# Kernel tuning notes

Measured on AMD Instinct MI355X. Metric: run time of the kernel, lower is better.

Reference implementation:

```python
import jax, jax.numpy as jnp
import numpy as np

B, S, E = 8, 2048, 768
N, H = 12, 64
INIT = 0.02
IGNORE = -100000.0


def setup_inputs() -> dict:
    key = jax.random.key(0)
    ks = jax.random.split(key, 5)
    return {
        "normalized_resid_pre": jax.random.normal(ks[0], (B, S, E), jnp.float32),
        "W_Q": jax.random.normal(ks[1], (N, E, H), jnp.float32) * INIT,
        "W_K": jax.random.normal(ks[2], (N, E, H), jnp.float32) * INIT,
        "W_V": jax.random.normal(ks[3], (N, E, H), jnp.float32) * INIT,
        "W_O": jax.random.normal(ks[4], (N, H, E), jnp.float32) * INIT,
        "b_Q": jnp.zeros((N, H), jnp.float32),
        "b_K": jnp.zeros((N, H), jnp.float32),
        "b_V": jnp.zeros((N, H), jnp.float32),
        "b_O": jnp.zeros((E,), jnp.float32),
    }


def reference(normalized_resid_pre, W_Q, W_K, W_V, W_O, b_Q, b_K, b_V, b_O):
    x = normalized_resid_pre
    b, s, e = x.shape
    d_head = W_Q.shape[-1]
    q = jnp.einsum('bse,neh->bsnh', x, W_Q) + b_Q  # [b, sq, n, h]
    k = jnp.einsum('bse,neh->bsnh', x, W_K) + b_K
    v = jnp.einsum('bse,neh->bsnh', x, W_V) + b_V
    scores = jnp.einsum('bqnh,bknh->bnqk', q, k) / jnp.sqrt(jnp.float32(d_head))
    mask = jnp.tril(jnp.ones((s, s), jnp.float32))  # [sq, sk]
    masked = mask * scores + (1.0 - mask) * IGNORE
    probs = jax.nn.softmax(masked, axis=-1)
    z = jnp.einsum('bnqk,bknh->bqnh', probs, v)
    # sum over heads of per-head output projection + bias
    out = jnp.einsum('bqnh,nhe->bqe', z, W_O) + b_O
    return out
```

## Files before the change

kernel.cpp:

```cpp
#include <hip/hip_runtime.h>
#include <hip/hip_bf16.h>
#include <stdint.h>


#define B_ 8
#define S_ 2048
#define E_ 768
#define NHEADS 12
#define HD 64
#define BS (B_*S_)
#define NHD (NHEADS*HD)

typedef short bf16x8 __attribute__((ext_vector_type(8)));
typedef short bf16x4 __attribute__((ext_vector_type(4)));
typedef float f32x4  __attribute__((ext_vector_type(4)));
typedef __hip_bfloat16 bf16;

typedef const __attribute__((address_space(1))) char* as1_t;
typedef __attribute__((address_space(3))) char* as3_t;

__device__ __forceinline__ f32x4 mfma16(bf16x8 a, bf16x8 b, f32x4 c) {
    return __builtin_amdgcn_mfma_f32_16x16x32_bf16(a, b, c, 0, 0, 0);
}
__device__ __forceinline__ bf16x8 ld8(const bf16* p) {
    return *reinterpret_cast<const bf16x8*>(p);
}
__device__ __forceinline__ void gload16(const bf16* g, bf16* l) {
    __builtin_amdgcn_global_load_lds((as1_t)g, (as3_t)l, 16, 0, 0);
}
__device__ __forceinline__ bf16x8 pack8(f32x4 a, f32x4 b) {
    union { bf16x8 v; __hip_bfloat162 h[4]; } u;
    u.h[0] = __float22bfloat162_rn(make_float2(a[0], a[1]));
    u.h[1] = __float22bfloat162_rn(make_float2(a[2], a[3]));
    u.h[2] = __float22bfloat162_rn(make_float2(b[0], b[1]));
    u.h[3] = __float22bfloat162_rn(make_float2(b[2], b[3]));
    return u.v;
}

__global__ __launch_bounds__(256) void prep_kernel(
    const float* __restrict__ x,  const float* __restrict__ Wq,
    const float* __restrict__ Wk, const float* __restrict__ Wv,
    const float* __restrict__ Wo,
    bf16* __restrict__ xb,  bf16* __restrict__ WqT, bf16* __restrict__ WkT,
    bf16* __restrict__ WvT, bf16* __restrict__ WoT)
{
    const int tid = blockIdx.x * 256 + threadIdx.x;
    const int nth = gridDim.x * 256;
    for (int i = tid; i < BS*E_; i += nth)
        xb[i] = __float2bfloat16(x[i]);
    for (int i = tid; i < NHD*E_; i += nth) {
        const int c = i / E_;
        const int e = i - c*E_;
        const int n = c >> 6, h = c & 63;
        const int src = (n*E_ + e)*HD + h;
        WqT[i] = __float2bfloat16(Wq[src]);
        WkT[i] = __float2bfloat16(Wk[src]);
        WvT[i] = __float2bfloat16(Wv[src]);
        WoT[e*NHD + c] = __float2bfloat16(Wo[i]);
    }
}


#define FENCE() asm volatile("" ::: "memory")
#define VMCNT3() asm volatile("s_waitcnt vmcnt(3)" ::: "memory")

#define A_ELEM(kh, rg) (((kh)*16 + (rg))*512)
#define B_ELEM(kh, rg) (((kh)*12 + (rg))*512)

#define STG_A(dst, gbase, kt, kh) do {                                            \
    const bf16* _s = (gbase) + (size_t)(l16)*768 + (kt)*64 + (kh)*32 + quad*8;    \
    gload16(_s + (size_t)(w*16)*768,     &(dst)[A_ELEM(kh, w)]);                  \
    gload16(_s + (size_t)((w+8)*16)*768, &(dst)[A_ELEM(kh, w+8)]);                \
} while (0)

#define STG_B(dst, gbase, kt) do {                                                \
    const bf16* _s = (gbase) + (size_t)(l16)*768 + (kt)*64 + quad*8;              \
    const int _k1 = (w < 4) ? 0 : 1;                                              \
    const int _r1 = (w < 4) ? (w + 8) : (w - 4);                                  \
    gload16(_s + (size_t)(w*16)*768,        &(dst)[B_ELEM(0, w)]);                \
    gload16(_s + (size_t)(_r1*16)*768 + _k1*32, &(dst)[B_ELEM(_k1, _r1)]);        \
    gload16(_s + (size_t)((w+4)*16)*768 + 32,   &(dst)[B_ELEM(1, w+4)]);          \
} while (0)

#define PHASE(bufA, bufB, q, LOADB, STAGE, WAIT) do {                             \
    if (LOADB) {                                                                  \
        _Pragma("unroll") for (int n = 0; n < 3; ++n)                             \
        _Pragma("unroll") for (int ks = 0; ks < 2; ++ks)                          \
            bfr[n][ks] = ld8(&(bufB)[((ks)*12 + wn*3 + n)*512 + lane*8]);         \
    }                                                                             \
    bf16x8 afr[2][2];                                                             \
    _Pragma("unroll") for (int m = 0; m < 2; ++m)                                 \
    _Pragma("unroll") for (int ks = 0; ks < 2; ++ks)                              \
        afr[m][ks] = ld8(&(bufA)[((ks)*16 + wm*8 + (q)*2 + m)*512 + lane*8]);     \
    STAGE;                                                                        \
    FENCE(); __builtin_amdgcn_s_barrier(); FENCE();                               \
    asm volatile("s_waitcnt lgkmcnt(0)" ::: "memory");                            \
    __builtin_amdgcn_s_setprio(1);                                                \
    _Pragma("unroll") for (int m = 0; m < 2; ++m)                                 \
    _Pragma("unroll") for (int n = 0; n < 3; ++n)                                 \
    _Pragma("unroll") for (int ks = 0; ks < 2; ++ks)                              \
        acc[(q)*2 + m][n] = mfma16(afr[m][ks], bfr[n][ks], acc[(q)*2 + m][n]);    \
    __builtin_amdgcn_s_setprio(0);                                                \
    WAIT;                                                                         \
    FENCE(); __builtin_amdgcn_s_barrier(); FENCE();                               \
} while (0)

#define GEMM192_BODY(Ab, Bb)                                                      \
    f32x4 acc[8][3];                                                              \
    _Pragma("unroll") for (int mf = 0; mf < 8; ++mf)                              \
    _Pragma("unroll") for (int nf = 0; nf < 3; ++nf)                              \
        acc[mf][nf] = (f32x4){0.f, 0.f, 0.f, 0.f};                                \
    bf16x8 bfr[3][2];                                                             \
    STG_A(sA0, Ab, 0, 0); STG_A(sA0, Ab, 0, 1);                                   \
    STG_B(sB0, Bb, 0);                                                            \
    STG_B(sB1, Bb, 1);                                                            \
    VMCNT3();                                                                     \
    FENCE(); __builtin_amdgcn_s_barrier(); FENCE();                               \
    _Pragma("unroll 1")                                                           \
    for (int i = 0; i < 6; ++i) {                                                 \
        const int kA  = 2*i + 1;                                                  \
        const int kN  = (2*i + 2 < 12) ? 2*i + 2 : 11;                            \
        const int kN3 = (2*i + 3 < 12) ? 2*i + 3 : 11;                            \
        PHASE(sA0, sB0, 0, 1, STG_A(sA1, Ab, kA, 0), (void)0);                    \
        PHASE(sA0, sB0, 1, 0, STG_A(sA1, Ab, kA, 1), (void)0);                    \
        PHASE(sA0, sB0, 2, 0, STG_B(sB0, Bb, kN),    (void)0);                    \
        PHASE(sA0, sB0, 3, 0, (void)0,               VMCNT3());                   \
        PHASE(sA1, sB1, 0, 1, STG_A(sA0, Ab, kN, 0), (void)0);                    \
        PHASE(sA1, sB1, 1, 0, STG_A(sA0, Ab, kN, 1), (void)0);                    \
        PHASE(sA1, sB1, 2, 0, STG_B(sB1, Bb, kN3),   (void)0);                    \
        PHASE(sA1, sB1, 3, 0, (void)0,               VMCNT3());                   \
    }                                                                             \
    asm volatile("s_waitcnt vmcnt(0)" ::: "memory");

__global__ __launch_bounds__(512, 2) void qkv_gemm256(
    const bf16* __restrict__ xb, const bf16* __restrict__ WT,
    const float* __restrict__ bq, const float* __restrict__ bk, const float* __restrict__ bv,
    bf16* __restrict__ Qb, bf16* __restrict__ Kb, bf16* __restrict__ VTb)
{
    __shared__ __align__(16) bf16 sA0[16384];
    __shared__ __align__(16) bf16 sA1[16384];
    __shared__ __align__(16) bf16 sB0[12288];
    __shared__ __align__(16) bf16 sB1[12288];

    const int tm = blockIdx.x, tn = blockIdx.y;
    const int lane = threadIdx.x & 63;
    const int w    = threadIdx.x >> 6;
    const int wm = w >> 2, wn = w & 3;
    const int l16 = lane & 15, quad = lane >> 4;
    const bf16* Ab = xb + (size_t)tm*256*E_;
    const bf16* Bb = WT + (size_t)tn*192*E_;

    GEMM192_BODY(Ab, Bb);

    const int mat = tn >> 2;
    const int cloc0 = (tn & 3)*192 + wn*48;
    const float* bias = (mat==0) ? bq : (mat==1) ? bk : bv;
    const float scale = (mat==0) ? 0.125f * 1.44269504088896340736f : 1.0f;
    bf16* dstQK = (mat==0) ? Qb : Kb;
    #pragma unroll
    for (int nf = 0; nf < 3; ++nf) {
        const int col = cloc0 + nf*16 + l16;
        const int hn = col >> 6, h = col & 63;
        const float bb = bias[col];
        #pragma unroll
        for (int mf = 0; mf < 8; ++mf) {
            const int row = tm*256 + wm*128 + mf*16 + quad*4;
            const int bi = row >> 11;
            const int s  = row & (S_-1);
            if (mat < 2) {
                bf16* d = dstQK + ((size_t)(bi*NHEADS + hn)*S_ + s)*HD + h;
                #pragma unroll
                for (int r = 0; r < 4; ++r)
                    d[(size_t)r*HD] = __float2bfloat16((acc[mf][nf][r] + bb)*scale);
            } else {
                bf16* d = VTb + ((size_t)(bi*NHEADS + hn)*HD + h)*S_ + s;
                union { bf16x4 v; bf16 e[4]; } u;
                #pragma unroll
                for (int r = 0; r < 4; ++r) u.e[r] = __float2bfloat16(acc[mf][nf][r] + bb);
                *reinterpret_cast<bf16x4*>(d) = u.v;
            }
        }
    }
}

__global__ __launch_bounds__(512, 2) void out_gemm256(
    const bf16* __restrict__ Z, const bf16* __restrict__ WoT,
    const float* __restrict__ bo, float* __restrict__ out)
{
    __shared__ __align__(16) bf16 sA0[16384];
    __shared__ __align__(16) bf16 sA1[16384];
    __shared__ __align__(16) bf16 sB0[12288];
    __shared__ __align__(16) bf16 sB1[12288];

    const int tm = blockIdx.x, tn = blockIdx.y;
    const int lane = threadIdx.x & 63;
    const int w    = threadIdx.x >> 6;
    const int wm = w >> 2, wn = w & 3;
    const int l16 = lane & 15, quad = lane >> 4;
    const bf16* Ab = Z   + (size_t)tm*256*NHD;
    const bf16* Bb = WoT + (size_t)tn*192*NHD;

    GEMM192_BODY(Ab, Bb);

    #pragma unroll
    for (int nf = 0; nf < 3; ++nf) {
        const int col = tn*192 + wn*48 + nf*16 + l16;
        const float bb = bo[col];
        #pragma unroll
        for (int mf = 0; mf < 8; ++mf) {
            const int row = tm*256 + wm*128 + mf*16 + quad*4;
            float* d = out + (size_t)row*E_ + col;
            #pragma unroll
            for (int r = 0; r < 4; ++r)
                d[(size_t)r*E_] = acc[mf][nf][r] + bb;
        }
    }
}

__global__ __launch_bounds__(256, 3) void attn_kernel(
    const bf16* __restrict__ Qb, const bf16* __restrict__ Kb,
    const bf16* __restrict__ VTb, bf16* __restrict__ Z)
{
    __shared__ __align__(16) bf16 sK[2][64*64];
    __shared__ __align__(16) bf16 sV[2][64*64];

    const int id = blockIdx.x;
    const int bx = id / 96;
    const int g  = id - bx*96;
    const int hn = g % NHEADS, b = g / NHEADS;
    const int tid  = threadIdx.x;
    const int w    = tid >> 6;
    const int lane = tid & 63;
    const int l16 = lane & 15, quad = lane >> 4;
    const size_t bn = (size_t)b*NHEADS + hn;

    const bf16* Qbase = Qb  + bn*S_*HD;
    const bf16* Kbase = Kb  + bn*S_*HD;
    const bf16* Vbase = VTb + bn*HD*S_;

    const int mA = tid, mB = tid + 256;
    const int rA = mA >> 3, cgA = mA & 7;
    const int rB = mB >> 3, cgB = mB & 7;
    const int slA = (rA*8 + ((cgA + rA + (rA>>3)) & 7)) * 8;
    const int slB = (rB*8 + ((cgB + rB + (rB>>3)) & 7)) * 8;
    const size_t vofA = (size_t)rA*S_ + cgA*8;
    const size_t vofB = (size_t)rB*S_ + cgB*8;

    const int kperm = (l16 >> 2)*8 + (l16 & 3);
    int kidx[2][2][2];
    #pragma unroll
    for (int c=0;c<2;c++)
        #pragma unroll
        for (int bg=0;bg<2;bg++)
            #pragma unroll
            for (int hf=0;hf<2;hf++) {
                const int r = 32*c + 4*bg + kperm;
                const int q = hf*4 + quad;
                kidx[c][bg][hf] = (r*8 + ((q + r + (r>>3)) & 7)) * 8;
            }
    int vidx[4][2];
    #pragma unroll
    for (int ht=0;ht<4;ht++)
        #pragma unroll
        for (int c=0;c<2;c++) {
            const int rho = ht*16 + l16;
            const int q = c*4 + quad;
            vidx[ht][c] = (rho*8 + ((q + rho + (rho>>3)) & 7)) * 8;
        }

    #pragma unroll
    for (int half = 0; half < 2; ++half) {
        const int qblk = half ? (S_/128 - 1 - bx) : bx;
        const int ktb  = 2*qblk + 1;
        const int ktw  = 2*qblk + (w >> 1);
        const int qbase = qblk*128 + w*32;

        bf16x8 bqf[2][2];
        #pragma unroll
        for (int qi=0;qi<2;qi++)
            #pragma unroll
            for (int hf=0;hf<2;hf++)
                bqf[qi][hf] = ld8(Qbase + (size_t)(qbase + qi*16 + l16)*HD + hf*32 + quad*8);

        f32x4 acc[2][4];
        #pragma unroll
        for (int qi=0;qi<2;qi++)
            #pragma unroll
            for (int ht=0;ht<4;ht++) acc[qi][ht] = (f32x4){0.f,0.f,0.f,0.f};
        float lsum[2] = {0.f, 0.f};

        bf16x8 k0 = ld8(Kbase + (size_t)mA*8);
        bf16x8 k1 = ld8(Kbase + (size_t)mB*8);
        bf16x8 v0 = ld8(Vbase + vofA);
        bf16x8 v1 = ld8(Vbase + vofB);
        *reinterpret_cast<bf16x8*>(&sK[0][slA]) = k0;
        *reinterpret_cast<bf16x8*>(&sK[0][slB]) = k1;
        *reinterpret_cast<bf16x8*>(&sV[0][slA]) = v0;
        *reinterpret_cast<bf16x8*>(&sV[0][slB]) = v1;
        __syncthreads();

        for (int kt = 0; kt <= ktb; ++kt) {
            if (kt < ktb) {
                const size_t kt1 = (size_t)(kt+1)*64;
                k0 = ld8(Kbase + kt1*HD + (size_t)mA*8);
                k1 = ld8(Kbase + kt1*HD + (size_t)mB*8);
                v0 = ld8(Vbase + vofA + kt1);
                v1 = ld8(Vbase + vofB + kt1);
            }
            if (kt <= ktw) {
                const bf16* kb = sK[kt & 1];
                const bf16* vb = sV[kt & 1];
                #pragma unroll
                for (int c=0;c<2;c++) {
                    const bf16x8 akA0 = ld8(kb + kidx[c][0][0]);
                    const bf16x8 akA1 = ld8(kb + kidx[c][0][1]);
                    const bf16x8 akB0 = ld8(kb + kidx[c][1][0]);
                    const bf16x8 akB1 = ld8(kb + kidx[c][1][1]);
                    bf16x8 av[4];
                    #pragma unroll
                    for (int ht=0;ht<4;ht++) av[ht] = ld8(vb + vidx[ht][c]);

                    #pragma unroll
                    for (int qi=0;qi<2;qi++) {
                        f32x4 s0 = (f32x4){0.f,0.f,0.f,0.f};
                        s0 = mfma16(akA0, bqf[qi][0], s0);
                        s0 = mfma16(akA1, bqf[qi][1], s0);
                        f32x4 s1 = (f32x4){0.f,0.f,0.f,0.f};
                        s1 = mfma16(akB0, bqf[qi][0], s1);
                        s1 = mfma16(akB1, bqf[qi][1], s1);
                        if (kt == ktw) {
                            const int q  = qbase + qi*16 + l16;
                            const int kb0 = kt*64 + c*32 + quad*8;
                            #pragma unroll
                            for (int r=0;r<4;r++) {
                                s0[r] = (kb0 + r     > q) ? -1e30f : s0[r];
                                s1[r] = (kb0 + 4 + r > q) ? -1e30f : s1[r];
                            }
                        }
                        float ls = 0.f;
                        #pragma unroll
                        for (int r=0;r<4;r++) {
                            s0[r] = __builtin_amdgcn_exp2f(s0[r]);
                            s1[r] = __builtin_amdgcn_exp2f(s1[r]);
                            ls += s0[r] + s1[r];
                        }
                        lsum[qi] += ls;
                        const bf16x8 pf = pack8(s0, s1);
                        #pragma unroll
                        for (int ht=0;ht<4;ht++)
                            acc[qi][ht] = mfma16(av[ht], pf, acc[qi][ht]);
                    }
                }
            }
            if (kt < ktb) {
                const int nb = (kt+1) & 1;
                *reinterpret_cast<bf16x8*>(&sK[nb][slA]) = k0;
                *reinterpret_cast<bf16x8*>(&sK[nb][slB]) = k1;
                *reinterpret_cast<bf16x8*>(&sV[nb][slA]) = v0;
                *reinterpret_cast<bf16x8*>(&sV[nb][slB]) = v1;
            }
            __syncthreads();
        }

        #pragma unroll
        for (int qi=0;qi<2;qi++) {
            float rs = lsum[qi];
            rs += __shfl_xor(rs, 16, 64);
            rs += __shfl_xor(rs, 32, 64);
            const float inv_l = 1.0f / rs;
            const int q = qbase + qi*16 + l16;
            bf16* zp = Z + ((size_t)b*S_ + q)*NHD + (size_t)hn*HD + quad*4;
            #pragma unroll
            for (int ht=0;ht<4;ht++) {
                union { bf16x4 v; bf16 e[4]; } u;
                #pragma unroll
                for (int r=0;r<4;r++) u.e[r] = __float2bfloat16(acc[qi][ht][r] * inv_l);
                *reinterpret_cast<bf16x4*>(zp + ht*16) = u.v;
            }
        }
    }
}

extern "C" void kernel_launch(void* const* d_in, const int* in_sizes, int n_in,
                              void* d_out, int out_size, void* d_ws, size_t ws_size,
                              hipStream_t stream)
{
    const float* x  = (const float*)d_in[0];
    const float* Wq = (const float*)d_in[1];
    const float* Wk = (const float*)d_in[2];
    const float* Wv = (const float*)d_in[3];
    const float* Wo = (const float*)d_in[4];
    const float* bq = (const float*)d_in[5];
    const float* bk = (const float*)d_in[6];
    const float* bv = (const float*)d_in[7];
    const float* bo = (const float*)d_in[8];
    float* out = (float*)d_out;

    char* ws = (char*)d_ws;
    size_t off = 0;
    auto alloc = [&](size_t bytes){ char* p = ws + off; off += (bytes + 255) & ~(size_t)255; return p; };
    bf16* xb  = (bf16*)alloc((size_t)BS*E_*2);
    bf16* WT  = (bf16*)alloc((size_t)3*NHD*E_*2);
    bf16* WoT = (bf16*)alloc((size_t)E_*NHD*2);
    bf16* Qb  = (bf16*)alloc((size_t)BS*NHD*2);
    bf16* Kb  = (bf16*)alloc((size_t)BS*NHD*2);
    bf16* VTb = (bf16*)alloc((size_t)BS*NHD*2);
    bf16* Zb  = (bf16*)alloc((size_t)BS*NHD*2);

    bf16* WqT = WT;
    bf16* WkT = WT + (size_t)NHD*E_;
    bf16* WvT = WT + (size_t)2*NHD*E_;

    prep_kernel<<<4096, 256, 0, stream>>>(x, Wq, Wk, Wv, Wo, xb, WqT, WkT, WvT, WoT);
    qkv_gemm256<<<dim3(BS/256, 12), 512, 0, stream>>>(xb, WT, bq, bk, bv, Qb, Kb, VTb);
    attn_kernel<<<768, 256, 0, stream>>>(Qb, Kb, VTb, Zb);
    out_gemm256<<<dim3(BS/256, E_/192), 512, 0, stream>>>(Zb, WoT, bo, out);
}
```

Before: 238.2 us.

## Triple-buffer A tiles in LDS to prefetch two K-steps ahead in GEMMs

```diff
diff --git a/kernel.cpp b/kernel.cpp
--- a/kernel.cpp
+++ b/kernel.cpp
@@ -62,7 +62,8 @@
 
 
 #define FENCE() asm volatile("" ::: "memory")
-#define VMCNT3() asm volatile("s_waitcnt vmcnt(3)" ::: "memory")
+#define VMCNT7() asm volatile("s_waitcnt vmcnt(7)" ::: "memory")
+#define MIN11(x) ((x) < 11 ? (x) : 11)
 
 #define A_ELEM(kh, rg) (((kh)*16 + (rg))*512)
 #define B_ELEM(kh, rg) (((kh)*12 + (rg))*512)
@@ -105,6 +106,16 @@
     FENCE(); __builtin_amdgcn_s_barrier(); FENCE();                               \
 } while (0)
 
+#define ITER8(r0, r1, w2, k0, Ab, Bb)                                             \
+    PHASE(r0, sB0, 0, 1, STG_A(w2, Ab, MIN11((k0)+2), 0), (void)0);               \
+    PHASE(r0, sB0, 1, 0, STG_A(w2, Ab, MIN11((k0)+2), 1), (void)0);               \
+    PHASE(r0, sB0, 2, 0, STG_B(sB0, Bb, MIN11((k0)+2)),   (void)0);               \
+    PHASE(r0, sB0, 3, 0, (void)0,                         VMCNT7());              \
+    PHASE(r1, sB1, 0, 1, STG_A(r0, Ab, MIN11((k0)+3), 0), (void)0);               \
+    PHASE(r1, sB1, 1, 0, STG_A(r0, Ab, MIN11((k0)+3), 1), (void)0);               \
+    PHASE(r1, sB1, 2, 0, STG_B(sB1, Bb, MIN11((k0)+3)),   (void)0);               \
+    PHASE(r1, sB1, 3, 0, (void)0,                         VMCNT7());
+
 #define GEMM192_BODY(Ab, Bb)                                                      \
     f32x4 acc[8][3];                                                              \
     _Pragma("unroll") for (int mf = 0; mf < 8; ++mf)                              \
@@ -113,22 +124,16 @@
     bf16x8 bfr[3][2];                                                             \
     STG_A(sA0, Ab, 0, 0); STG_A(sA0, Ab, 0, 1);                                   \
     STG_B(sB0, Bb, 0);                                                            \
+    STG_A(sA1, Ab, 1, 0); STG_A(sA1, Ab, 1, 1);                                   \
     STG_B(sB1, Bb, 1);                                                            \
-    VMCNT3();                                                                     \
+    VMCNT7();                                                                     \
     FENCE(); __builtin_amdgcn_s_barrier(); FENCE();                               \
     _Pragma("unroll 1")                                                           \
-    for (int i = 0; i < 6; ++i) {                                                 \
-        const int kA  = 2*i + 1;                                                  \
-        const int kN  = (2*i + 2 < 12) ? 2*i + 2 : 11;                            \
-        const int kN3 = (2*i + 3 < 12) ? 2*i + 3 : 11;                            \
-        PHASE(sA0, sB0, 0, 1, STG_A(sA1, Ab, kA, 0), (void)0);                    \
-        PHASE(sA0, sB0, 1, 0, STG_A(sA1, Ab, kA, 1), (void)0);                    \
-        PHASE(sA0, sB0, 2, 0, STG_B(sB0, Bb, kN),    (void)0);                    \
-        PHASE(sA0, sB0, 3, 0, (void)0,               VMCNT3());                   \
-        PHASE(sA1, sB1, 0, 1, STG_A(sA0, Ab, kN, 0), (void)0);                    \
-        PHASE(sA1, sB1, 1, 0, STG_A(sA0, Ab, kN, 1), (void)0);                    \
-        PHASE(sA1, sB1, 2, 0, STG_B(sB1, Bb, kN3),   (void)0);                    \
-        PHASE(sA1, sB1, 3, 0, (void)0,               VMCNT3());                   \
+    for (int ii = 0; ii < 2; ++ii) {                                              \
+        const int k0 = 6*ii;                                                      \
+        ITER8(sA0, sA1, sA2, k0+0, Ab, Bb)                                        \
+        ITER8(sA2, sA0, sA1, k0+2, Ab, Bb)                                        \
+        ITER8(sA1, sA2, sA0, k0+4, Ab, Bb)                                        \
     }                                                                             \
     asm volatile("s_waitcnt vmcnt(0)" ::: "memory");
 
@@ -139,6 +144,7 @@
 {
     __shared__ __align__(16) bf16 sA0[16384];
     __shared__ __align__(16) bf16 sA1[16384];
+    __shared__ __align__(16) bf16 sA2[16384];
     __shared__ __align__(16) bf16 sB0[12288];
     __shared__ __align__(16) bf16 sB1[12288];
 
@@ -189,6 +195,7 @@
 {
     __shared__ __align__(16) bf16 sA0[16384];
     __shared__ __align__(16) bf16 sA1[16384];
+    __shared__ __align__(16) bf16 sA2[16384];
     __shared__ __align__(16) bf16 sB0[12288];
     __shared__ __align__(16) bf16 sB1[12288];
 
```

Result: faster. 232.2 us (-2.5%).

## Shrink GEMM M-tile to 128 and simplify pipeline to per-k-tile double buffering

Applied to the files above, without the earlier changes.

```diff
diff --git a/kernel.cpp b/kernel.cpp
--- a/kernel.cpp
+++ b/kernel.cpp
@@ -62,15 +62,18 @@
 
 
 #define FENCE() asm volatile("" ::: "memory")
-#define VMCNT3() asm volatile("s_waitcnt vmcnt(3)" ::: "memory")
-
-#define A_ELEM(kh, rg) (((kh)*16 + (rg))*512)
+#define LGKM0() do { asm volatile("s_waitcnt lgkmcnt(0)" ::: "memory"); \
+                     __builtin_amdgcn_sched_barrier(0); } while (0)
+#define VMCNT0() asm volatile("s_waitcnt vmcnt(0)" ::: "memory")
+#define MIN11(x) ((x) < 11 ? (x) : 11)
+
+#define A_ELEM(kh, rg) (((kh)*8 + (rg))*512)
 #define B_ELEM(kh, rg) (((kh)*12 + (rg))*512)
 
-#define STG_A(dst, gbase, kt, kh) do {                                            \
-    const bf16* _s = (gbase) + (size_t)(l16)*768 + (kt)*64 + (kh)*32 + quad*8;    \
-    gload16(_s + (size_t)(w*16)*768,     &(dst)[A_ELEM(kh, w)]);                  \
-    gload16(_s + (size_t)((w+8)*16)*768, &(dst)[A_ELEM(kh, w+8)]);                \
+#define STG_A(dst, gbase, kt) do {                                                \
+    const bf16* _s = (gbase) + (size_t)(w*16 + l16)*768 + (kt)*64 + quad*8;       \
+    gload16(_s,      &(dst)[A_ELEM(0, w)]);                                       \
+    gload16(_s + 32, &(dst)[A_ELEM(1, w)]);                                       \
 } while (0)
 
 #define STG_B(dst, gbase, kt) do {                                                \
@@ -82,63 +85,67 @@
     gload16(_s + (size_t)((w+4)*16)*768 + 32,   &(dst)[B_ELEM(1, w+4)]);          \
 } while (0)
 
-#define PHASE(bufA, bufB, q, LOADB, STAGE, WAIT) do {                             \
-    if (LOADB) {                                                                  \
+#define KTILE(bufA, bufB, nA, nB, ktn, Ab, Bb) do {                               \
+                                          \
+    _Pragma("unroll") for (int n = 0; n < 3; ++n)                                 \
+    _Pragma("unroll") for (int ks = 0; ks < 2; ++ks)                              \
+        bfr[n][ks] = ld8(&(bufB)[((ks)*12 + wn*3 + n)*512 + lane*8]);             \
+    {                                                                             \
+        bf16x8 afr[2][2];                                                         \
+        _Pragma("unroll") for (int m = 0; m < 2; ++m)                             \
+        _Pragma("unroll") for (int ks = 0; ks < 2; ++ks)                          \
+            afr[m][ks] = ld8(&(bufA)[((ks)*8 + wm*4 + m)*512 + lane*8]);          \
+        STG_A(nA, Ab, ktn);                                                       \
+        LGKM0();                                                                  \
+        __builtin_amdgcn_s_setprio(1);                                            \
+        _Pragma("unroll") for (int m = 0; m < 2; ++m)                             \
         _Pragma("unroll") for (int n = 0; n < 3; ++n)                             \
         _Pragma("unroll") for (int ks = 0; ks < 2; ++ks)                          \
-            bfr[n][ks] = ld8(&(bufB)[((ks)*12 + wn*3 + n)*512 + lane*8]);         \
+            acc[m][n] = mfma16(afr[m][ks], bfr[n][ks], acc[m][n]);                \
+        __builtin_amdgcn_s_setprio(0);                                            \
     }                                                                             \
-    bf16x8 afr[2][2];                                                             \
-    _Pragma("unroll") for (int m = 0; m < 2; ++m)                                 \
-    _Pragma("unroll") for (int ks = 0; ks < 2; ++ks)                              \
-        afr[m][ks] = ld8(&(bufA)[((ks)*16 + wm*8 + (q)*2 + m)*512 + lane*8]);     \
-    STAGE;                                                                        \
-    FENCE(); __builtin_amdgcn_s_barrier(); FENCE();                               \
-    asm volatile("s_waitcnt lgkmcnt(0)" ::: "memory");                            \
-    __builtin_amdgcn_s_setprio(1);                                                \
-    _Pragma("unroll") for (int m = 0; m < 2; ++m)                                 \
-    _Pragma("unroll") for (int n = 0; n < 3; ++n)                                 \
-    _Pragma("unroll") for (int ks = 0; ks < 2; ++ks)                              \
-        acc[(q)*2 + m][n] = mfma16(afr[m][ks], bfr[n][ks], acc[(q)*2 + m][n]);    \
-    __builtin_amdgcn_s_setprio(0);                                                \
-    WAIT;                                                                         \
+                                                    \
+    {                                                                             \
+        bf16x8 afr[2][2];                                                         \
+        _Pragma("unroll") for (int m = 0; m < 2; ++m)                             \
+        _Pragma("unroll") for (int ks = 0; ks < 2; ++ks)                          \
+            afr[m][ks] = ld8(&(bufA)[((ks)*8 + wm*4 + 2 + m)*512 + lane*8]);      \
+        STG_B(nB, Bb, ktn);                                                       \
+        LGKM0();                                                                  \
+        __builtin_amdgcn_s_setprio(1);                                            \
+        _Pragma("unroll") for (int m = 0; m < 2; ++m)                             \
+        _Pragma("unroll") for (int n = 0; n < 3; ++n)                             \
+        _Pragma("unroll") for (int ks = 0; ks < 2; ++ks)                          \
+            acc[2+m][n] = mfma16(afr[m][ks], bfr[n][ks], acc[2+m][n]);            \
+        __builtin_amdgcn_s_setprio(0);                                            \
+    }                                                                             \
+    VMCNT0();                                                                     \
     FENCE(); __builtin_amdgcn_s_barrier(); FENCE();                               \
 } while (0)
 
-#define GEMM192_BODY(Ab, Bb)                                                      \
-    f32x4 acc[8][3];                                                              \
-    _Pragma("unroll") for (int mf = 0; mf < 8; ++mf)                              \
+#define GEMM128_BODY(Ab, Bb)                                                      \
+    f32x4 acc[4][3];                                                              \
+    _Pragma("unroll") for (int mf = 0; mf < 4; ++mf)                              \
     _Pragma("unroll") for (int nf = 0; nf < 3; ++nf)                              \
         acc[mf][nf] = (f32x4){0.f, 0.f, 0.f, 0.f};                                \
     bf16x8 bfr[3][2];                                                             \
-    STG_A(sA0, Ab, 0, 0); STG_A(sA0, Ab, 0, 1);                                   \
-    STG_B(sB0, Bb, 0);                                                            \
-    STG_B(sB1, Bb, 1);                                                            \
-    VMCNT3();                                                                     \
+    STG_A(sA0, Ab, 0); STG_B(sB0, Bb, 0);                                         \
+    VMCNT0();                                                                     \
     FENCE(); __builtin_amdgcn_s_barrier(); FENCE();                               \
     _Pragma("unroll 1")                                                           \
-    for (int i = 0; i < 6; ++i) {                                                 \
-        const int kA  = 2*i + 1;                                                  \
-        const int kN  = (2*i + 2 < 12) ? 2*i + 2 : 11;                            \
-        const int kN3 = (2*i + 3 < 12) ? 2*i + 3 : 11;                            \
-        PHASE(sA0, sB0, 0, 1, STG_A(sA1, Ab, kA, 0), (void)0);                    \
-        PHASE(sA0, sB0, 1, 0, STG_A(sA1, Ab, kA, 1), (void)0);                    \
-        PHASE(sA0, sB0, 2, 0, STG_B(sB0, Bb, kN),    (void)0);                    \
-        PHASE(sA0, sB0, 3, 0, (void)0,               VMCNT3());                   \
-        PHASE(sA1, sB1, 0, 1, STG_A(sA0, Ab, kN, 0), (void)0);                    \
-        PHASE(sA1, sB1, 1, 0, STG_A(sA0, Ab, kN, 1), (void)0);                    \
-        PHASE(sA1, sB1, 2, 0, STG_B(sB1, Bb, kN3),   (void)0);                    \
-        PHASE(sA1, sB1, 3, 0, (void)0,               VMCNT3());                   \
-    }                                                                             \
-    asm volatile("s_waitcnt vmcnt(0)" ::: "memory");
-
-__global__ __launch_bounds__(512, 2) void qkv_gemm256(
+    for (int i2 = 0; i2 < 6; ++i2) {                                              \
+        const int kt0 = 2*i2;                                                     \
+        KTILE(sA0, sB0, sA1, sB1, kt0 + 1,        Ab, Bb);                        \
+        KTILE(sA1, sB1, sA0, sB0, MIN11(kt0 + 2), Ab, Bb);                        \
+    }
+
+__global__ __launch_bounds__(512, 4) void qkv_gemm256(
     const bf16* __restrict__ xb, const bf16* __restrict__ WT,
     const float* __restrict__ bq, const float* __restrict__ bk, const float* __restrict__ bv,
     bf16* __restrict__ Qb, bf16* __restrict__ Kb, bf16* __restrict__ VTb)
 {
-    __shared__ __align__(16) bf16 sA0[16384];
-    __shared__ __align__(16) bf16 sA1[16384];
+    __shared__ __align__(16) bf16 sA0[8192];
+    __shared__ __align__(16) bf16 sA1[8192];
     __shared__ __align__(16) bf16 sB0[12288];
     __shared__ __align__(16) bf16 sB1[12288];
 
@@ -147,10 +154,10 @@
     const int w    = threadIdx.x >> 6;
     const int wm = w >> 2, wn = w & 3;
     const int l16 = lane & 15, quad = lane >> 4;
-    const bf16* Ab = xb + (size_t)tm*256*E_;
+    const bf16* Ab = xb + (size_t)tm*128*E_;
     const bf16* Bb = WT + (size_t)tn*192*E_;
 
-    GEMM192_BODY(Ab, Bb);
+    GEMM128_BODY(Ab, Bb);
 
     const int mat = tn >> 2;
     const int cloc0 = (tn & 3)*192 + wn*48;
@@ -163,8 +170,8 @@
         const int hn = col >> 6, h = col & 63;
         const float bb = bias[col];
         #pragma unroll
-        for (int mf = 0; mf < 8; ++mf) {
-            const int row = tm*256 + wm*128 + mf*16 + quad*4;
+        for (int mf = 0; mf < 4; ++mf) {
+            const int row = tm*128 + wm*64 + mf*16 + quad*4;
             const int bi = row >> 11;
             const int s  = row & (S_-1);
             if (mat < 2) {
@@ -183,12 +190,12 @@
     }
 }
 
-__global__ __launch_bounds__(512, 2) void out_gemm256(
+__global__ __launch_bounds__(512, 4) void out_gemm256(
     const bf16* __restrict__ Z, const bf16* __restrict__ WoT,
     const float* __restrict__ bo, float* __restrict__ out)
 {
-    __shared__ __align__(16) bf16 sA0[16384];
-    __shared__ __align__(16) bf16 sA1[16384];
+    __shared__ __align__(16) bf16 sA0[8192];
+    __shared__ __align__(16) bf16 sA1[8192];
     __shared__ __align__(16) bf16 sB0[12288];
     __shared__ __align__(16) bf16 sB1[12288];
 
@@ -197,18 +204,18 @@
     const int w    = threadIdx.x >> 6;
     const int wm = w >> 2, wn = w & 3;
     const int l16 = lane & 15, quad = lane >> 4;
-    const bf16* Ab = Z   + (size_t)tm*256*NHD;
+    const bf16* Ab = Z   + (size_t)tm*128*NHD;
     const bf16* Bb = WoT + (size_t)tn*192*NHD;
 
-    GEMM192_BODY(Ab, Bb);
+    GEMM128_BODY(Ab, Bb);
 
     #pragma unroll
     for (int nf = 0; nf < 3; ++nf) {
         const int col = tn*192 + wn*48 + nf*16 + l16;
         const float bb = bo[col];
         #pragma unroll
-        for (int mf = 0; mf < 8; ++mf) {
-            const int row = tm*256 + wm*128 + mf*16 + quad*4;
+        for (int mf = 0; mf < 4; ++mf) {
+            const int row = tm*128 + wm*64 + mf*16 + quad*4;
             float* d = out + (size_t)row*E_ + col;
             #pragma unroll
             for (int r = 0; r < 4; ++r)
@@ -412,7 +419,7 @@
     bf16* WvT = WT + (size_t)2*NHD*E_;
 
     prep_kernel<<<4096, 256, 0, stream>>>(x, Wq, Wk, Wv, Wo, xb, WqT, WkT, WvT, WoT);
-    qkv_gemm256<<<dim3(BS/256, 12), 512, 0, stream>>>(xb, WT, bq, bk, bv, Qb, Kb, VTb);
+    qkv_gemm256<<<dim3(BS/128, 12), 512, 0, stream>>>(xb, WT, bq, bk, bv, Qb, Kb, VTb);
     attn_kernel<<<768, 256, 0, stream>>>(Qb, Kb, VTb, Zb);
-    out_gemm256<<<dim3(BS/256, E_/192), 512, 0, stream>>>(Zb, WoT, bo, out);
-}
+    out_gemm256<<<dim3(BS/128, E_/192), 512, 0, stream>>>(Zb, WoT, bo, out);
+}
```

Measured after the change: 242.5 us. No clear change (+1.8%).
